# Optimization experiments

Measured on AMD Instinct MI355X. Metric: run time of the kernel, lower is better.

## Reference

```python
import jax, jax.numpy as jnp
import numpy as np

DILATIONS = (1, 2, 4, 8)
NUM_ITER = 10
W1 = 0.3
W2 = 0.01
# 3x3 neighborhood excluding center, row-major (matches get_kernel ordering)
OFFS = ((0, 0), (0, 1), (0, 2), (1, 0), (1, 2), (2, 0), (2, 1), (2, 2))
# distance weights: sqrt(2) for diagonals (indices 0,2,5,7), 1 otherwise
POS_VALS = np.array([np.sqrt(2), 1.0, np.sqrt(2), 1.0, 1.0, np.sqrt(2), 1.0, np.sqrt(2)], dtype=np.float32)


def dilated_neighbors(x):
    # x: [b, c, h, w] -> [b, c, K, h, w], K = 8 * len(DILATIONS)
    b, c, h, w = x.shape
    outs = []
    for d in DILATIONS:
        xp = jnp.pad(x, ((0, 0), (0, 0), (d, d), (d, d)), mode='edge')
        for di, dj in OFFS:
            outs.append(jax.lax.dynamic_slice(xp, (0, 0, di * d, dj * d), (b, c, h, w)))
    return jnp.stack(outs, axis=2)


def pos_vec():
    # [K] concatenation of POS_VALS * d for each dilation
    return jnp.concatenate([jnp.asarray(POS_VALS) * d for d in DILATIONS], axis=0)


def setup_inputs() -> dict:
    key = jax.random.key(0)
    k1, k2 = jax.random.split(key)
    imgs = jax.random.normal(k1, (8, 3, 128, 128), dtype=jnp.float32)
    masks = jax.random.uniform(k2, (8, 21, 128, 128), dtype=jnp.float32)
    return {"imgs": imgs, "masks": masks}


def reference(imgs, masks):
    # pixel affinity: [b, 1, K, h, w]
    nb = dilated_neighbors(imgs)                                  # [b,c,K,h,w]
    diff = jnp.abs(nb - imgs[:, :, None, :, :])
    std = jnp.std(nb, axis=2, ddof=1, keepdims=True)              # unbiased, like torch.std
    aff = -((diff / (std + 1e-8) / W1) ** 2).mean(axis=1, keepdims=True)

    # position affinity: constant over b,h,w -> compute on the [K] vector
    pos = pos_vec()                                               # [K]
    pos_std = jnp.std(pos, ddof=1)
    pos_aff = -((pos / (pos_std + 1e-8) / W1) ** 2)

    aff = jax.nn.softmax(aff, axis=2) + W2 * jax.nn.softmax(pos_aff)[None, None, :, None, None]

    for _ in range(NUM_ITER):
        masks = (dilated_neighbors(masks) * aff).sum(axis=2)
    return masks
```

## Files before the change

kernel.cpp:

```cpp
#include <hip/hip_runtime.h>
#include <cmath>

#define B_   8
#define CI_  3
#define CM_  21
#define H_   128
#define W_   128
#define K_   32
#define PAD_ 8
#define PW_  144
#define PH_  144
#define NC_  3

typedef float f4 __attribute__((ext_vector_type(4)));
typedef _Float16 h4 __attribute__((ext_vector_type(4)));
typedef _Float16 h8v __attribute__((ext_vector_type(8)));

struct PosSoft { float v[K_]; };

template<int S>
__device__ __forceinline__ f4 shw(f4 A, f4 B) {
  if constexpr (S == 0) return A;
  else if constexpr (S == 1) return (f4){A.y, A.z, A.w, B.x};
  else if constexpr (S == 2) return (f4){A.z, A.w, B.x, B.y};
  else                       return (f4){A.w, B.x, B.y, B.z};
}

__device__ __forceinline__ f4 ldh(const _Float16* p, int off) {
  return __builtin_convertvector(*reinterpret_cast<const h4*>(p + off), f4);
}

__global__ __launch_bounds__(128) void aff_kernel(const float* __restrict__ imgs,
                                                  _Float16* __restrict__ aff,
                                                  PosSoft ps) {
  constexpr int OI[8] = {-1,-1,-1, 0, 0, 1, 1, 1};
  constexpr int OJ[8] = {-1, 0, 1,-1, 1,-1, 0, 1};
  const int j = threadIdx.x;
  const int i = blockIdx.x;
  const int b = blockIdx.y;
  const float* img = imgs + (size_t)b * CI_ * H_ * W_;

  float ctr[CI_];
#pragma unroll
  for (int c = 0; c < CI_; ++c) ctr[c] = img[c * H_ * W_ + i * W_ + j];

  float s[CI_] = {0.f, 0.f, 0.f}, s2[CI_] = {0.f, 0.f, 0.f};
#pragma unroll
  for (int k = 0; k < K_; ++k) {
    const int d  = 1 << (k >> 3);
    const int ci = min(max(i + OI[k & 7] * d, 0), H_ - 1);
    const int cj = min(max(j + OJ[k & 7] * d, 0), W_ - 1);
#pragma unroll
    for (int c = 0; c < CI_; ++c) {
      float v = img[c * H_ * W_ + ci * W_ + cj];
      s[c] += v; s2[c] += v * v;
    }
  }

  float inv[CI_];
#pragma unroll
  for (int c = 0; c < CI_; ++c) {
    float mean = s[c] * (1.f / K_);
    float var  = (s2[c] - (float)K_ * mean * mean) * (1.f / (K_ - 1));
    var = fmaxf(var, 0.f);
    inv[c] = 1.f / ((sqrtf(var) + 1e-8f) * 0.3f);
  }

  float araw[K_];
#pragma unroll
  for (int k = 0; k < K_; ++k) {
    const int d  = 1 << (k >> 3);
    const int ci = min(max(i + OI[k & 7] * d, 0), H_ - 1);
    const int cj = min(max(j + OJ[k & 7] * d, 0), W_ - 1);
    float t = 0.f;
#pragma unroll
    for (int c = 0; c < CI_; ++c) {
      float v  = img[c * H_ * W_ + ci * W_ + cj];
      float dd = fabsf(v - ctr[c]) * inv[c];
      t += dd * dd;
    }
    araw[k] = -t * (1.f / CI_);
  }

  float m = araw[0];
#pragma unroll
  for (int k = 1; k < K_; ++k) m = fmaxf(m, araw[k]);
  float sum = 0.f;
#pragma unroll
  for (int k = 0; k < K_; ++k) { float e = __expf(araw[k] - m); araw[k] = e; sum += e; }
  const float rs = 1.f / sum;

  _Float16* ap = aff + ((size_t)(b * H_ + i) * K_) * W_ + j;
#pragma unroll
  for (int k = 0; k < K_; ++k) ap[k * W_] = (_Float16)(araw[k] * rs + ps.v[k]);
}

__global__ void pad_kernel(const float* __restrict__ src, _Float16* __restrict__ dst,
                           int total4) {
  int idx = blockIdx.x * blockDim.x + threadIdx.x;
  if (idx >= total4) return;
  int q  = idx % (PW_ / 4);
  int t  = idx / (PW_ / 4);
  int pi = t % PH_;
  int p  = t / PH_;
  int i = min(max(pi - PAD_, 0), H_ - 1);
  const float* srow = src + (size_t)p * (H_ * W_) + i * W_;
  h4 o;
#pragma unroll
  for (int e = 0; e < 4; ++e) {
    int j = min(max(q * 4 + e - PAD_, 0), W_ - 1);
    o[e] = (_Float16)srow[j];
  }
  *reinterpret_cast<h4*>(dst + (size_t)p * (PH_ * PW_) + pi * PW_ + q * 4) = o;
}

#define LX(C, DR, CO) (lb + ((C) * 2880 + ((DR) + 8) * 144 + ((CO) + 8)))
#define LDS4(IDX) __builtin_convertvector(*reinterpret_cast<const h4*>(&sm[(IDX)]), f4)

#define HCH(C, ACC) do {                                                       \
    f4 m2 = LDS4(LX(C, 0, -8)), m1 = LDS4(LX(C, 0, -4));                       \
    f4 c0 = LDS4(LX(C, 0, 0)),  c1 = LDS4(LX(C, 0, 4));                        \
    f4 c2 = LDS4(LX(C, 0, 8));                                                 \
    ACC += h1m * shw<3>(m1, c0) + h1p * shw<1>(c0, c1);                        \
    ACC += h2m * shw<2>(m1, c0) + h2p * shw<2>(c0, c1);                        \
    ACC += h4m * m1 + h4p * c1;                                                \
    ACC += h8m * m2 + h8p * c2;                                                \
  } while (0)

#define VCHS(D, SM, C, ACC) do {                                               \
    f4 ua = LDS4(LX(C, -(D), -4)), ub = LDS4(LX(C, -(D), 0));                  \
    f4 uc = LDS4(LX(C, -(D), 4));                                              \
    ACC += A0 * shw<SM>(ua, ub) + A1 * ub + A2 * shw<D>(ub, uc);               \
    f4 da = LDS4(LX(C, (D), -4)), db = LDS4(LX(C, (D), 0));                    \
    f4 dc = LDS4(LX(C, (D), 4));                                               \
    ACC += A5 * shw<SM>(da, db) + A6 * db + A7 * shw<D>(db, dc);               \
  } while (0)

#define VCH4(C, ACC) do {                                                      \
    f4 ua = LDS4(LX(C, -4, -4)), ub = LDS4(LX(C, -4, 0)), uc = LDS4(LX(C, -4, 4)); \
    ACC += A0 * ua + A1 * ub + A2 * uc;                                        \
    f4 da = LDS4(LX(C, 4, -4)), db = LDS4(LX(C, 4, 0)), dc = LDS4(LX(C, 4, 4)); \
    ACC += A5 * da + A6 * db + A7 * dc;                                        \
  } while (0)

#define VCH8(C, ACC) do {                                                      \
    f4 ua = LDS4(LX(C, -8, -8)), ub = LDS4(LX(C, -8, 0)), uc = LDS4(LX(C, -8, 8)); \
    ACC += A0 * ua + A1 * ub + A2 * uc;                                        \
    f4 da = LDS4(LX(C, 8, -8)), db = LDS4(LX(C, 8, 0)), dc = LDS4(LX(C, 8, 8)); \
    ACC += A5 * da + A6 * db + A7 * dc;                                        \
  } while (0)

#define AFFV(AB)                                                               \
    f4 A0 = ldh(AB, 0),      A1 = ldh(AB, W_),     A2 = ldh(AB, 2 * W_);       \
    f4 A5 = ldh(AB, 5 * W_), A6 = ldh(AB, 6 * W_), A7 = ldh(AB, 7 * W_);

template <int PADOUT>
__global__ __launch_bounds__(128, 3) void iter_kernel(const _Float16* __restrict__ src,
                                                      const _Float16* __restrict__ aff,
                                                      void* __restrict__ dstv) {
  __shared__ _Float16 sm[NC_ * 20 * PW_];

  const int bid  = blockIdx.x;
  const int b    = bid & 7;
  const int t    = bid >> 3;
  const int grp  = t % 7;
  const int tile = t / 7;

  const int tid = threadIdx.x;
  const int qx  = tid & 31;
  const int j0  = qx * 4;
  const int tr  = tid >> 5;
  const int i   = tile * 4 + tr;
  const int i0  = tile * 4;
  const int c0  = grp * NC_;

  constexpr int CHP = PH_ * PW_;

  {
    const _Float16* pl = src + (size_t)(b * CM_ + c0) * CHP + (size_t)i0 * PW_;
    for (int s = tid; s < 1080; s += 128) {
      int c = s / 360;
      int r = s - c * 360;
      h8v v = *reinterpret_cast<const h8v*>(pl + (size_t)c * CHP + r * 8);
      *reinterpret_cast<h8v*>(&sm[c * 2880 + r * 8]) = v;
    }
  }
  __syncthreads();

  const int lb = tr * PW_ + j0;

  const _Float16* ab0 = aff + ((size_t)(b * H_ + i) * K_) * W_ + j0;
  const _Float16* ab1 = ab0 +  8 * W_;
  const _Float16* ab2 = ab0 + 16 * W_;
  const _Float16* ab3 = ab0 + 24 * W_;

  f4 acc0 = (f4){0.f, 0.f, 0.f, 0.f};
  f4 acc1 = (f4){0.f, 0.f, 0.f, 0.f};
  f4 acc2 = (f4){0.f, 0.f, 0.f, 0.f};

  {
    f4 h1m = ldh(ab0, 3 * W_), h1p = ldh(ab0, 4 * W_);
    f4 h2m = ldh(ab1, 3 * W_), h2p = ldh(ab1, 4 * W_);
    f4 h4m = ldh(ab2, 3 * W_), h4p = ldh(ab2, 4 * W_);
    f4 h8m = ldh(ab3, 3 * W_), h8p = ldh(ab3, 4 * W_);
    HCH(0, acc0);
    HCH(1, acc1);
    HCH(2, acc2);
  }
  {
    AFFV(ab0);
    VCHS(1, 3, 0, acc0);
    VCHS(1, 3, 1, acc1);
    VCHS(1, 3, 2, acc2);
  }
  {
    AFFV(ab1);
    VCHS(2, 2, 0, acc0);
    VCHS(2, 2, 1, acc1);
    VCHS(2, 2, 2, acc2);
  }
  {
    AFFV(ab2);
    VCH4(0, acc0);
    VCH4(1, acc1);
    VCH4(2, acc2);
  }
  {
    AFFV(ab3);
    VCH8(0, acc0);
    VCH8(1, acc1);
    VCH8(2, acc2);
  }

  if (PADOUT) {
    _Float16* d0 = (_Float16*)dstv + (size_t)(b * CM_ + c0) * CHP;
    _Float16* d1 = d0 + CHP;
    _Float16* d2 = d0 + 2 * CHP;
    h4 o0 = __builtin_convertvector(acc0, h4);
    h4 o1 = __builtin_convertvector(acc1, h4);
    h4 o2 = __builtin_convertvector(acc2, h4);
    const int pr = i + PAD_;
    const int r0 = (i == 0)      ? 0         : pr;
    const int r1 = (i == H_ - 1) ? (PH_ - 1) : pr;
    for (int r = r0; r <= r1; ++r) {
      _Float16* row0 = d0 + r * PW_;
      _Float16* row1 = d1 + r * PW_;
      _Float16* row2 = d2 + r * PW_;
      *reinterpret_cast<h4*>(row0 + PAD_ + j0) = o0;
      *reinterpret_cast<h4*>(row1 + PAD_ + j0) = o1;
      *reinterpret_cast<h4*>(row2 + PAD_ + j0) = o2;
      if (qx == 0) {
        h4 s0 = (h4){o0.x, o0.x, o0.x, o0.x};
        h4 s1 = (h4){o1.x, o1.x, o1.x, o1.x};
        h4 s2 = (h4){o2.x, o2.x, o2.x, o2.x};
        *reinterpret_cast<h4*>(row0) = s0; *reinterpret_cast<h4*>(row0 + 4) = s0;
        *reinterpret_cast<h4*>(row1) = s1; *reinterpret_cast<h4*>(row1 + 4) = s1;
        *reinterpret_cast<h4*>(row2) = s2; *reinterpret_cast<h4*>(row2 + 4) = s2;
      }
      if (qx == 31) {
        h4 s0 = (h4){o0.w, o0.w, o0.w, o0.w};
        h4 s1 = (h4){o1.w, o1.w, o1.w, o1.w};
        h4 s2 = (h4){o2.w, o2.w, o2.w, o2.w};
        *reinterpret_cast<h4*>(row0 + PW_ - 8) = s0; *reinterpret_cast<h4*>(row0 + PW_ - 4) = s0;
        *reinterpret_cast<h4*>(row1 + PW_ - 8) = s1; *reinterpret_cast<h4*>(row1 + PW_ - 4) = s1;
        *reinterpret_cast<h4*>(row2 + PW_ - 8) = s2; *reinterpret_cast<h4*>(row2 + PW_ - 4) = s2;
      }
    }
  } else {
    float* dc = (float*)dstv + (size_t)(b * CM_ + c0) * (H_ * W_) + (size_t)i * W_ + j0;
    *reinterpret_cast<f4*>(dc)                 = acc0;
    *reinterpret_cast<f4*>(dc + (H_ * W_))     = acc1;
    *reinterpret_cast<f4*>(dc + 2 * (H_ * W_)) = acc2;
  }
}

extern "C" void kernel_launch(void* const* d_in, const int* in_sizes, int n_in,
                              void* d_out, int out_size, void* d_ws, size_t ws_size,
                              hipStream_t stream) {
  const float* imgs  = (const float*)d_in[0];
  const float* masks = (const float*)d_in[1];
  float* out = (float*)d_out;

  char* ws = (char*)d_ws;
  const size_t affBytes = (size_t)B_ * K_ * H_ * W_ * sizeof(_Float16);
  const size_t padBytes = (size_t)B_ * CM_ * PH_ * PW_ * sizeof(_Float16);
  _Float16* aff = (_Float16*)ws;
  _Float16* P0  = (_Float16*)(ws + affBytes);
  _Float16* P1  = (_Float16*)(ws + affBytes + padBytes);

  PosSoft ps;
  {
    const double pv[8] = {1.4142135623730951, 1.0, 1.4142135623730951, 1.0,
                          1.0, 1.4142135623730951, 1.0, 1.4142135623730951};
    double pos[K_];
    for (int di = 0; di < 4; ++di) {
      double d = (double)(1 << di);
      for (int o = 0; o < 8; ++o) pos[di * 8 + o] = pv[o] * d;
    }
    double mean = 0; for (int k = 0; k < K_; ++k) mean += pos[k]; mean /= K_;
    double var = 0;  for (int k = 0; k < K_; ++k) { double dd = pos[k] - mean; var += dd * dd; }
    var /= (K_ - 1);
    double sd = sqrt(var);
    double pa[K_]; double m = -1e300;
    for (int k = 0; k < K_; ++k) {
      double r = pos[k] / ((sd + 1e-8) * 0.3);
      pa[k] = -(r * r);
      if (pa[k] > m) m = pa[k];
    }
    double es = 0; for (int k = 0; k < K_; ++k) { pa[k] = exp(pa[k] - m); es += pa[k]; }
    for (int k = 0; k < K_; ++k) ps.v[k] = (float)(0.01 * pa[k] / es);
  }

  aff_kernel<<<dim3(H_, B_), 128, 0, stream>>>(imgs, aff, ps);

  const int total4 = B_ * CM_ * PH_ * (PW_ / 4);
  pad_kernel<<<(total4 + 255) / 256, 256, 0, stream>>>(masks, P0, total4);

  const int nblk = B_ * 7 * (H_ / 4);
  _Float16* s = P0;
  _Float16* d = P1;
  for (int it = 0; it < 9; ++it) {
    iter_kernel<1><<<nblk, 128, 0, stream>>>(s, aff, (void*)d);
    _Float16* tm = s; s = d; d = tm;
  }
  iter_kernel<0><<<nblk, 128, 0, stream>>>(s, aff, (void*)out);
}
```

Measured before the change: 150.4 us.

## Compute stencil in packed fp16 and prefetch all affinities before LDS fill

The iteration kernel now does its multiply-accumulate in half precision (h4 vectors) instead of converting every LDS and affinity load to fp32. This removes many conversion instructions and allows packed fp16 math. All 32 affinity vectors are now loaded up front, before the shared-memory staging loop, so their global latency overlaps the tile copy. The risks are lower accumulation precision over 32 terms and 10 iterations, and higher register pressure from holding 32 h4 values under launch bounds (128,3).

```diff
diff --git a/kernel.cpp b/kernel.cpp
--- a/kernel.cpp
+++ b/kernel.cpp
@@ -19,15 +19,12 @@
 struct PosSoft { float v[K_]; };
 
 template<int S>
-__device__ __forceinline__ f4 shw(f4 A, f4 B) {
-  if constexpr (S == 0) return A;
-  else if constexpr (S == 1) return (f4){A.y, A.z, A.w, B.x};
-  else if constexpr (S == 2) return (f4){A.z, A.w, B.x, B.y};
-  else                       return (f4){A.w, B.x, B.y, B.z};
-}
-
-__device__ __forceinline__ f4 ldh(const _Float16* p, int off) {
-  return __builtin_convertvector(*reinterpret_cast<const h4*>(p + off), f4);
+__device__ __forceinline__ h4 shwh(h4 A, h4 B) {
+  return __builtin_shufflevector(A, B, S, S + 1, S + 2, S + 3);
+}
+
+__device__ __forceinline__ h4 lda(const _Float16* p, int off) {
+  return *reinterpret_cast<const h4*>(p + off);
 }
 
 __global__ __launch_bounds__(128) void aff_kernel(const float* __restrict__ imgs,
@@ -115,44 +112,40 @@
 }
 
 #define LX(C, DR, CO) (lb + ((C) * 2880 + ((DR) + 8) * 144 + ((CO) + 8)))
-#define LDS4(IDX) __builtin_convertvector(*reinterpret_cast<const h4*>(&sm[(IDX)]), f4)
+#define LDSH(IDX) (*reinterpret_cast<const h4*>(&sm[(IDX)]))
 
 #define HCH(C, ACC) do {                                                       \
-    f4 m2 = LDS4(LX(C, 0, -8)), m1 = LDS4(LX(C, 0, -4));                       \
-    f4 c0 = LDS4(LX(C, 0, 0)),  c1 = LDS4(LX(C, 0, 4));                        \
-    f4 c2 = LDS4(LX(C, 0, 8));                                                 \
-    ACC += h1m * shw<3>(m1, c0) + h1p * shw<1>(c0, c1);                        \
-    ACC += h2m * shw<2>(m1, c0) + h2p * shw<2>(c0, c1);                        \
-    ACC += h4m * m1 + h4p * c1;                                                \
-    ACC += h8m * m2 + h8p * c2;                                                \
+    h4 m2 = LDSH(LX(C, 0, -8)), m1 = LDSH(LX(C, 0, -4));                       \
+    h4 c0 = LDSH(LX(C, 0, 0)),  c1 = LDSH(LX(C, 0, 4));                        \
+    h4 c2 = LDSH(LX(C, 0, 8));                                                 \
+    ACC += a03 * shwh<3>(m1, c0) + a04 * shwh<1>(c0, c1);                      \
+    ACC += a13 * shwh<2>(m1, c0) + a14 * shwh<2>(c0, c1);                      \
+    ACC += a23 * m1 + a24 * c1;                                                \
+    ACC += a33 * m2 + a34 * c2;                                                \
   } while (0)
 
-#define VCHS(D, SM, C, ACC) do {                                               \
-    f4 ua = LDS4(LX(C, -(D), -4)), ub = LDS4(LX(C, -(D), 0));                  \
-    f4 uc = LDS4(LX(C, -(D), 4));                                              \
-    ACC += A0 * shw<SM>(ua, ub) + A1 * ub + A2 * shw<D>(ub, uc);               \
-    f4 da = LDS4(LX(C, (D), -4)), db = LDS4(LX(C, (D), 0));                    \
-    f4 dc = LDS4(LX(C, (D), 4));                                               \
-    ACC += A5 * shw<SM>(da, db) + A6 * db + A7 * shw<D>(db, dc);               \
+#define VCHS(D, SM, A0, A1, A2, A5, A6, A7, C, ACC) do {                       \
+    h4 ua = LDSH(LX(C, -(D), -4)), ub = LDSH(LX(C, -(D), 0));                  \
+    h4 uc = LDSH(LX(C, -(D), 4));                                              \
+    ACC += A0 * shwh<SM>(ua, ub) + A1 * ub + A2 * shwh<D>(ub, uc);             \
+    h4 da = LDSH(LX(C, (D), -4)), db = LDSH(LX(C, (D), 0));                    \
+    h4 dc = LDSH(LX(C, (D), 4));                                               \
+    ACC += A5 * shwh<SM>(da, db) + A6 * db + A7 * shwh<D>(db, dc);             \
   } while (0)
 
-#define VCH4(C, ACC) do {                                                      \
-    f4 ua = LDS4(LX(C, -4, -4)), ub = LDS4(LX(C, -4, 0)), uc = LDS4(LX(C, -4, 4)); \
+#define VCH4(A0, A1, A2, A5, A6, A7, C, ACC) do {                              \
+    h4 ua = LDSH(LX(C, -4, -4)), ub = LDSH(LX(C, -4, 0)), uc = LDSH(LX(C, -4, 4)); \
     ACC += A0 * ua + A1 * ub + A2 * uc;                                        \
-    f4 da = LDS4(LX(C, 4, -4)), db = LDS4(LX(C, 4, 0)), dc = LDS4(LX(C, 4, 4)); \
+    h4 da = LDSH(LX(C, 4, -4)), db = LDSH(LX(C, 4, 0)), dc = LDSH(LX(C, 4, 4)); \
     ACC += A5 * da + A6 * db + A7 * dc;                                        \
   } while (0)
 
-#define VCH8(C, ACC) do {                                                      \
-    f4 ua = LDS4(LX(C, -8, -8)), ub = LDS4(LX(C, -8, 0)), uc = LDS4(LX(C, -8, 8)); \
+#define VCH8(A0, A1, A2, A5, A6, A7, C, ACC) do {                              \
+    h4 ua = LDSH(LX(C, -8, -8)), ub = LDSH(LX(C, -8, 0)), uc = LDSH(LX(C, -8, 8)); \
     ACC += A0 * ua + A1 * ub + A2 * uc;                                        \
-    f4 da = LDS4(LX(C, 8, -8)), db = LDS4(LX(C, 8, 0)), dc = LDS4(LX(C, 8, 8)); \
+    h4 da = LDSH(LX(C, 8, -8)), db = LDSH(LX(C, 8, 0)), dc = LDSH(LX(C, 8, 8)); \
     ACC += A5 * da + A6 * db + A7 * dc;                                        \
   } while (0)
-
-#define AFFV(AB)                                                               \
-    f4 A0 = ldh(AB, 0),      A1 = ldh(AB, W_),     A2 = ldh(AB, 2 * W_);       \
-    f4 A5 = ldh(AB, 5 * W_), A6 = ldh(AB, 6 * W_), A7 = ldh(AB, 7 * W_);
 
 template <int PADOUT>
 __global__ __launch_bounds__(128, 3) void iter_kernel(const _Float16* __restrict__ src,
@@ -176,6 +169,20 @@
 
   constexpr int CHP = PH_ * PW_;
 
+  const _Float16* ab = aff + ((size_t)(b * H_ + i) * K_) * W_ + j0;
+  h4 a00 = lda(ab,  0 * W_), a01 = lda(ab,  1 * W_), a02 = lda(ab,  2 * W_),
+     a03 = lda(ab,  3 * W_), a04 = lda(ab,  4 * W_), a05 = lda(ab,  5 * W_),
+     a06 = lda(ab,  6 * W_), a07 = lda(ab,  7 * W_);
+  h4 a10 = lda(ab,  8 * W_), a11 = lda(ab,  9 * W_), a12 = lda(ab, 10 * W_),
+     a13 = lda(ab, 11 * W_), a14 = lda(ab, 12 * W_), a15 = lda(ab, 13 * W_),
+     a16 = lda(ab, 14 * W_), a17 = lda(ab, 15 * W_);
+  h4 a20 = lda(ab, 16 * W_), a21 = lda(ab, 17 * W_), a22 = lda(ab, 18 * W_),
+     a23 = lda(ab, 19 * W_), a24 = lda(ab, 20 * W_), a25 = lda(ab, 21 * W_),
+     a26 = lda(ab, 22 * W_), a27 = lda(ab, 23 * W_);
+  h4 a30 = lda(ab, 24 * W_), a31 = lda(ab, 25 * W_), a32 = lda(ab, 26 * W_),
+     a33 = lda(ab, 27 * W_), a34 = lda(ab, 28 * W_), a35 = lda(ab, 29 * W_),
+     a36 = lda(ab, 30 * W_), a37 = lda(ab, 31 * W_);
+
   {
     const _Float16* pl = src + (size_t)(b * CM_ + c0) * CHP + (size_t)i0 * PW_;
     for (int s = tid; s < 1080; s += 128) {
@@ -189,56 +196,32 @@
 
   const int lb = tr * PW_ + j0;
 
-  const _Float16* ab0 = aff + ((size_t)(b * H_ + i) * K_) * W_ + j0;
-  const _Float16* ab1 = ab0 +  8 * W_;
-  const _Float16* ab2 = ab0 + 16 * W_;
-  const _Float16* ab3 = ab0 + 24 * W_;
-
-  f4 acc0 = (f4){0.f, 0.f, 0.f, 0.f};
-  f4 acc1 = (f4){0.f, 0.f, 0.f, 0.f};
-  f4 acc2 = (f4){0.f, 0.f, 0.f, 0.f};
-
-  {
-    f4 h1m = ldh(ab0, 3 * W_), h1p = ldh(ab0, 4 * W_);
-    f4 h2m = ldh(ab1, 3 * W_), h2p = ldh(ab1, 4 * W_);
-    f4 h4m = ldh(ab2, 3 * W_), h4p = ldh(ab2, 4 * W_);
-    f4 h8m = ldh(ab3, 3 * W_), h8p = ldh(ab3, 4 * W_);
-    HCH(0, acc0);
-    HCH(1, acc1);
-    HCH(2, acc2);
-  }
-  {
-    AFFV(ab0);
-    VCHS(1, 3, 0, acc0);
-    VCHS(1, 3, 1, acc1);
-    VCHS(1, 3, 2, acc2);
-  }
-  {
-    AFFV(ab1);
-    VCHS(2, 2, 0, acc0);
-    VCHS(2, 2, 1, acc1);
-    VCHS(2, 2, 2, acc2);
-  }
-  {
-    AFFV(ab2);
-    VCH4(0, acc0);
-    VCH4(1, acc1);
-    VCH4(2, acc2);
-  }
-  {
-    AFFV(ab3);
-    VCH8(0, acc0);
-    VCH8(1, acc1);
-    VCH8(2, acc2);
-  }
+  h4 acc0 = (h4){0, 0, 0, 0};
+  h4 acc1 = (h4){0, 0, 0, 0};
+  h4 acc2 = (h4){0, 0, 0, 0};
+
+  HCH(0, acc0); HCH(1, acc1); HCH(2, acc2);
+
+  VCHS(1, 3, a00, a01, a02, a05, a06, a07, 0, acc0);
+  VCHS(1, 3, a00, a01, a02, a05, a06, a07, 1, acc1);
+  VCHS(1, 3, a00, a01, a02, a05, a06, a07, 2, acc2);
+
+  VCHS(2, 2, a10, a11, a12, a15, a16, a17, 0, acc0);
+  VCHS(2, 2, a10, a11, a12, a15, a16, a17, 1, acc1);
+  VCHS(2, 2, a10, a11, a12, a15, a16, a17, 2, acc2);
+
+  VCH4(a20, a21, a22, a25, a26, a27, 0, acc0);
+  VCH4(a20, a21, a22, a25, a26, a27, 1, acc1);
+  VCH4(a20, a21, a22, a25, a26, a27, 2, acc2);
+
+  VCH8(a30, a31, a32, a35, a36, a37, 0, acc0);
+  VCH8(a30, a31, a32, a35, a36, a37, 1, acc1);
+  VCH8(a30, a31, a32, a35, a36, a37, 2, acc2);
 
   if (PADOUT) {
     _Float16* d0 = (_Float16*)dstv + (size_t)(b * CM_ + c0) * CHP;
     _Float16* d1 = d0 + CHP;
     _Float16* d2 = d0 + 2 * CHP;
-    h4 o0 = __builtin_convertvector(acc0, h4);
-    h4 o1 = __builtin_convertvector(acc1, h4);
-    h4 o2 = __builtin_convertvector(acc2, h4);
     const int pr = i + PAD_;
     const int r0 = (i == 0)      ? 0         : pr;
     const int r1 = (i == H_ - 1) ? (PH_ - 1) : pr;
@@ -246,21 +229,21 @@
       _Float16* row0 = d0 + r * PW_;
       _Float16* row1 = d1 + r * PW_;
       _Float16* row2 = d2 + r * PW_;
-      *reinterpret_cast<h4*>(row0 + PAD_ + j0) = o0;
-      *reinterpret_cast<h4*>(row1 + PAD_ + j0) = o1;
-      *reinterpret_cast<h4*>(row2 + PAD_ + j0) = o2;
+      *reinterpret_cast<h4*>(row0 + PAD_ + j0) = acc0;
+      *reinterpret_cast<h4*>(row1 + PAD_ + j0) = acc1;
+      *reinterpret_cast<h4*>(row2 + PAD_ + j0) = acc2;
       if (qx == 0) {
-        h4 s0 = (h4){o0.x, o0.x, o0.x, o0.x};
-        h4 s1 = (h4){o1.x, o1.x, o1.x, o1.x};
-        h4 s2 = (h4){o2.x, o2.x, o2.x, o2.x};
+        h4 s0 = (h4){acc0.x, acc0.x, acc0.x, acc0.x};
+        h4 s1 = (h4){acc1.x, acc1.x, acc1.x, acc1.x};
+        h4 s2 = (h4){acc2.x, acc2.x, acc2.x, acc2.x};
         *reinterpret_cast<h4*>(row0) = s0; *reinterpret_cast<h4*>(row0 + 4) = s0;
         *reinterpret_cast<h4*>(row1) = s1; *reinterpret_cast<h4*>(row1 + 4) = s1;
         *reinterpret_cast<h4*>(row2) = s2; *reinterpret_cast<h4*>(row2 + 4) = s2;
       }
       if (qx == 31) {
-        h4 s0 = (h4){o0.w, o0.w, o0.w, o0.w};
-        h4 s1 = (h4){o1.w, o1.w, o1.w, o1.w};
-        h4 s2 = (h4){o2.w, o2.w, o2.w, o2.w};
+        h4 s0 = (h4){acc0.w, acc0.w, acc0.w, acc0.w};
+        h4 s1 = (h4){acc1.w, acc1.w, acc1.w, acc1.w};
+        h4 s2 = (h4){acc2.w, acc2.w, acc2.w, acc2.w};
         *reinterpret_cast<h4*>(row0 + PW_ - 8) = s0; *reinterpret_cast<h4*>(row0 + PW_ - 4) = s0;
         *reinterpret_cast<h4*>(row1 + PW_ - 8) = s1; *reinterpret_cast<h4*>(row1 + PW_ - 4) = s1;
         *reinterpret_cast<h4*>(row2 + PW_ - 8) = s2; *reinterpret_cast<h4*>(row2 + PW_ - 4) = s2;
@@ -268,9 +251,9 @@
     }
   } else {
     float* dc = (float*)dstv + (size_t)(b * CM_ + c0) * (H_ * W_) + (size_t)i * W_ + j0;
-    *reinterpret_cast<f4*>(dc)                 = acc0;
-    *reinterpret_cast<f4*>(dc + (H_ * W_))     = acc1;
-    *reinterpret_cast<f4*>(dc + 2 * (H_ * W_)) = acc2;
+    *reinterpret_cast<f4*>(dc)                 = __builtin_convertvector(acc0, f4);
+    *reinterpret_cast<f4*>(dc + (H_ * W_))     = __builtin_convertvector(acc1, f4);
+    *reinterpret_cast<f4*>(dc + 2 * (H_ * W_)) = __builtin_convertvector(acc2, f4);
   }
 }
 
```

New measurement: 132.2 us. -12.1%, faster.
